# Kernel tuning notes

Hardware: AMD Instinct MI355X
Metric: run time of the kernel (lower is better)

## Reference

```python
import jax, jax.numpy as jnp
import numpy as np

B, S, D = 2, 2048, 2048
H, HKV, HD = 16, 2, 128
THETA = 10000.0


def setup_inputs() -> dict:
    key = jax.random.key(0)
    ks = jax.random.split(key, 5)
    x = jax.random.normal(ks[0], (B, S, D), jnp.float32)
    Wq = jax.random.normal(ks[1], (D, H * HD), jnp.float32) * 0.02
    Wk = jax.random.normal(ks[2], (D, HKV * HD), jnp.float32) * 0.02
    Wv = jax.random.normal(ks[3], (D, HKV * HD), jnp.float32) * 0.02
    Wo = jax.random.normal(ks[4], (H * HD, D), jnp.float32) * 0.02
    mask = jnp.tril(jnp.ones((S, S), jnp.int32))[None, None]  # causal [1,1,S,S]
    return {"x": x, "mask": mask, "Wq": Wq, "Wk": Wk, "Wv": Wv, "Wo": Wo}


def _rope(t, seq_len):
    # t: [B, S, H, HD]; matches RotaryPositionalEmbedding (cos/sin broadcast [S,1,HD])
    inv_freq = 1.0 / (THETA ** (jnp.arange(0, HD, 2, dtype=jnp.float32) / HD))
    pos = jnp.arange(seq_len, dtype=jnp.float32)
    freqs = jnp.einsum('i,j->ij', pos, inv_freq)          # [S, HD/2]
    emb = jnp.concatenate([freqs, freqs], axis=-1)        # [S, HD]
    cos = jnp.cos(emb)[:, None, :]
    sin = jnp.sin(emb)[:, None, :]
    x1, x2 = jnp.split(t, 2, axis=-1)
    rot = jnp.concatenate([-x2, x1], axis=-1)             # rotate_half
    return t * cos + rot * sin


def reference(x, mask, Wq, Wk, Wv, Wo):
    Bx, Sx, _ = x.shape
    q = (x @ Wq).reshape(Bx, Sx, H, HD)
    k = (x @ Wk).reshape(Bx, Sx, HKV, HD)
    v = (x @ Wv).reshape(Bx, Sx, HKV, HD)
    q = _rope(q, Sx)
    k = _rope(k, Sx)
    rep = H // HKV
    # torch .repeat along head dim == tiling (not interleaved)
    k = jnp.tile(k, (1, 1, rep, 1))  # [B, S, H, HD]
    v = jnp.tile(v, (1, 1, rep, 1))
    scale = 1.0 / np.sqrt(HD).astype(np.float32)
    scores = jnp.einsum('bqhd,bkhd->bhqk', q, k) * scale  # [B, H, S, S]
    scores = jnp.where(mask == 0, -jnp.inf, scores)
    attn = jax.nn.softmax(scores.astype(jnp.float32), axis=-1).astype(scores.dtype)
    out = jnp.einsum('bhqk,bkhd->bqhd', attn, v).reshape(Bx, Sx, H * HD)
    return out @ Wo
```

## Files before the change

### kernel.cpp

```cpp
#include <hip/hip_runtime.h>
#include <hip/hip_bf16.h>

#define S_LEN 2048
#define DMODEL 2048
#define NHEAD 16
#define NKVH 2
#define HDIM 128
#define NROW 4096
#define NQKV 2560
#define SCALE 0.08838834764831845f

using short8 = __attribute__((ext_vector_type(8))) short;
using bf16x8 = __attribute__((ext_vector_type(8))) __bf16;
using f32x4  = __attribute__((ext_vector_type(4))) float;

__device__ __forceinline__ f32x4 mfma16(short8 a, short8 b, f32x4 c) {
  return __builtin_amdgcn_mfma_f32_16x16x32_bf16(
      __builtin_bit_cast(bf16x8, a), __builtin_bit_cast(bf16x8, b), c, 0, 0, 0);
}

__device__ __forceinline__ void gload_lds16(const void* g, void* l) {
  __builtin_amdgcn_global_load_lds(
      (const __attribute__((address_space(1))) unsigned int*)g,
      (__attribute__((address_space(3))) unsigned int*)l, 16, 0, 0);
}

__device__ __forceinline__ void storeC(float* C, long idx, float v) { C[idx] = v; }
__device__ __forceinline__ void storeC(__hip_bfloat16* C, long idx, float v) {
  C[idx] = __float2bfloat16(v);
}

__device__ __forceinline__ unsigned short bf16bits(float f) {
  __hip_bfloat16 h = __float2bfloat16(f);
  return *(unsigned short*)&h;
}

__global__ void conv_x(const float* __restrict__ x, __hip_bfloat16* __restrict__ xb) {
  long i = ((long)blockIdx.x * 256 + threadIdx.x) * 4;
  float4 v = *(const float4*)(x + i);
  __hip_bfloat16 o[4];
  o[0] = __float2bfloat16(v.x); o[1] = __float2bfloat16(v.y);
  o[2] = __float2bfloat16(v.z); o[3] = __float2bfloat16(v.w);
  *(ushort4*)(xb + i) = *(const ushort4*)o;
}

__global__ void convT3(const float* __restrict__ Wq, const float* __restrict__ Wk,
                       const float* __restrict__ Wv, __hip_bfloat16* __restrict__ dst) {
  __shared__ float t[32][33];
  int nt = blockIdx.x, kt = blockIdx.y;
  int tx = threadIdx.x, ty = threadIdx.y;
  const float* src; int Ns, n0, row_off;
  if (nt < 64)      { src = Wq; Ns = 2048; n0 = nt * 32;        row_off = n0; }
  else if (nt < 72) { src = Wk; Ns = 256;  n0 = (nt - 64) * 32; row_off = 2048 + n0; }
  else              { src = Wv; Ns = 256;  n0 = (nt - 72) * 32; row_off = 2304 + n0; }
#pragma unroll
  for (int i = 0; i < 4; i++)
    t[ty + i * 8][tx] = src[(long)(kt * 32 + ty + i * 8) * Ns + n0 + tx];
  __syncthreads();
#pragma unroll
  for (int i = 0; i < 4; i++)
    dst[(long)(row_off + ty + i * 8) * 2048 + kt * 32 + tx] =
        __float2bfloat16(t[tx][ty + i * 8]);
}

__global__ void convT(const float* __restrict__ src, __hip_bfloat16* __restrict__ dst,
                      int Ns, int row_off) {
  __shared__ float t[32][33];
  int nt = blockIdx.x, kt = blockIdx.y;
  int tx = threadIdx.x, ty = threadIdx.y;
#pragma unroll
  for (int i = 0; i < 4; i++)
    t[ty + i * 8][tx] = src[(long)(kt * 32 + ty + i * 8) * Ns + nt * 32 + tx];
  __syncthreads();
#pragma unroll
  for (int i = 0; i < 4; i++)
    dst[(long)(row_off + nt * 32 + ty + i * 8) * 2048 + kt * 32 + tx] =
        __float2bfloat16(t[tx][ty + i * 8]);
}

__global__ void mk_table(float* __restrict__ cost, float* __restrict__ sint) {
  int i = blockIdx.x * 256 + threadIdx.x;
  int s = i >> 6, j = i & 63;
  double f = pow(10000.0, -(double)j / 64.0);
  double a = (double)s * f;
  cost[i] = (float)cos(a);
  sint[i] = (float)sin(a);
}

template <typename OutT>
__global__ void gemm_bt(const __hip_bfloat16* __restrict__ A,
                        const __hip_bfloat16* __restrict__ Bt,
                        OutT* __restrict__ C, int M, int N, int K) {
  __shared__ __align__(16) __hip_bfloat16 a_lds[128 * 32];
  __shared__ __align__(16) __hip_bfloat16 b_lds[128 * 32];
  const int tid = threadIdx.x;
  const int wid = tid >> 6, lane = tid & 63;
  const int m0 = blockIdx.y * 128, n0 = blockIdx.x * 128;
  const int wr = wid >> 1, wc = wid & 1;
  const int lrow = lane & 15, lk = lane >> 4;

  const __hip_bfloat16* ag0 = A + (long)(m0 + wid * 16 + (lane >> 2)) * K + (lane & 3) * 8;
  const __hip_bfloat16* bg0 = Bt + (long)(n0 + wid * 16 + (lane >> 2)) * K + (lane & 3) * 8;
  char* al = (char*)a_lds + wid * 1024 + lane * 16;
  char* bl = (char*)b_lds + wid * 1024 + lane * 16;

  f32x4 acc[4][4] = {};

  for (int k0 = 0; k0 < K; k0 += 32) {
    gload_lds16(ag0 + k0, al);
    gload_lds16(ag0 + 64 * (long)K + k0, al + 4096);
    gload_lds16(bg0 + k0, bl);
    gload_lds16(bg0 + 64 * (long)K + k0, bl + 4096);
    __syncthreads();
    short8 af[4], bfr[4];
#pragma unroll
    for (int mi = 0; mi < 4; mi++)
      af[mi] = *(const short8*)(a_lds + (wr * 64 + mi * 16 + lrow) * 32 + lk * 8);
#pragma unroll
    for (int ni = 0; ni < 4; ni++)
      bfr[ni] = *(const short8*)(b_lds + (wc * 64 + ni * 16 + lrow) * 32 + lk * 8);
#pragma unroll
    for (int mi = 0; mi < 4; mi++)
#pragma unroll
      for (int ni = 0; ni < 4; ni++)
        acc[mi][ni] = mfma16(af[mi], bfr[ni], acc[mi][ni]);
    __syncthreads();
  }
#pragma unroll
  for (int mi = 0; mi < 4; mi++)
#pragma unroll
    for (int ni = 0; ni < 4; ni++)
#pragma unroll
      for (int r = 0; r < 4; r++) {
        long row = m0 + wr * 64 + mi * 16 + lk * 4 + r;
        long col = n0 + wc * 64 + ni * 16 + lrow;
        storeC(C, row * N + col, acc[mi][ni][r]);
      }
}

__global__ void rope_kernel(const __hip_bfloat16* __restrict__ qkv,
                            const float* __restrict__ cost, const float* __restrict__ sint,
                            __hip_bfloat16* __restrict__ q_r, __hip_bfloat16* __restrict__ k_t) {
  int tid = threadIdx.x;
  long row = (long)blockIdx.x * 4 + (tid >> 6);
  int j = tid & 63;
  int hh = (int)(row % 18);
  long bs = row / 18;
  int s = (int)(bs & (S_LEN - 1));
  int b = (int)(bs >> 11);
  const __hip_bfloat16* src = qkv + bs * NQKV;
  float c = cost[s * 64 + j], sn = sint[s * 64 + j];
  if (hh < NHEAD) {
    int col0 = hh * HDIM;
    float lo = __bfloat162float(src[col0 + j]);
    float hi = __bfloat162float(src[col0 + j + 64]);
    __hip_bfloat16* dst = q_r + ((long)(b * NHEAD + hh) * S_LEN + s) * HDIM;
    dst[j]      = __float2bfloat16((lo * c - hi * sn) * SCALE);
    dst[j + 64] = __float2bfloat16((hi * c + lo * sn) * SCALE);
  } else {
    int kvh = hh - NHEAD;
    int col0 = DMODEL + kvh * HDIM;
    float lo = __bfloat162float(src[col0 + j]);
    float hi = __bfloat162float(src[col0 + j + 64]);
    long tb = (long)(b * NKVH + kvh) * (S_LEN * HDIM) + (long)(s >> 5) * 4096 +
              (s & 15) * 8 + (j & 7);
    int cs4 = ((s >> 4) & 1) * 4;
    int lkq = ((j >> 3) & 3) * 16;
    int dch = j >> 5;
    k_t[tb + (long)((cs4 + dch) * 64 + lkq) * 8]     = __float2bfloat16(lo * c - hi * sn);
    k_t[tb + (long)((cs4 + dch + 2) * 64 + lkq) * 8] = __float2bfloat16(hi * c + lo * sn);
  }
}

__global__ void vtrans(const __hip_bfloat16* __restrict__ qkv, __hip_bfloat16* __restrict__ v_t) {
  __shared__ __hip_bfloat16 t[32][33];
  int st = blockIdx.x, dt = blockIdx.y, bk = blockIdx.z;
  int tx = threadIdx.x, ty = threadIdx.y;
#pragma unroll
  for (int i = 0; i < 4; i++)
    t[ty + i * 8][tx] = qkv[((long)(bk >> 1) * S_LEN + st * 32 + ty + i * 8) * NQKV +
                            DMODEL + NKVH * HDIM + (bk & 1) * HDIM + dt * 32 + tx];
  __syncthreads();
  long base = (long)bk * (S_LEN * HDIM) + (long)st * 4096 + (tx >> 3) * 128 + (tx & 7);
#pragma unroll
  for (int i = 0; i < 4; i++) {
    int d = dt * 32 + ty + i * 8;
    v_t[base + (long)((d >> 4) * 64 + (d & 15)) * 8] = t[tx][ty + i * 8];
  }
}

__global__ __launch_bounds__(512, 2) void attn_kernel(
    const __hip_bfloat16* __restrict__ q_r, const __hip_bfloat16* __restrict__ k_t,
    const __hip_bfloat16* __restrict__ v_t, __hip_bfloat16* __restrict__ attn_a) {
  __shared__ __align__(16) __hip_bfloat16 k_st[2][4096];
  __shared__ __align__(16) __hip_bfloat16 v_st[2][4096];
  __shared__ __align__(16) __hip_bfloat16 p_lds[8][2 * 16 * 40];
  const int tid = threadIdx.x;
  const int wid = tid >> 6, lane = tid & 63;
  const int lrow = lane & 15, lk = lane >> 4;
  const int bidx = blockIdx.x;
  const int pr = bidx & 31;
  const int hg = (bidx >> 5) & 1;
  const int kv = (bidx >> 6) & 1;
  const int b = bidx >> 7;
  const int myc = (wid < 4) ? pr : (63 - pr);
  const int h = kv + 2 * (hg * 4 + (wid & 3));
  const int q0 = myc * 32;
  const int nkt_w = myc + 1;
  const int nkt_max = 64 - pr;

  const __hip_bfloat16* qb = q_r + (long)(b * NHEAD + h) * S_LEN * HDIM;
  const __hip_bfloat16* kbase = k_t + (long)(b * NKVH + kv) * (S_LEN * HDIM);
  const __hip_bfloat16* vbase = v_t + (long)(b * NKVH + kv) * (S_LEN * HDIM);

  char* kd0 = (char*)&k_st[0][0] + tid * 16;
  char* kd1 = (char*)&k_st[1][0] + tid * 16;
  char* vd0 = (char*)&v_st[0][0] + tid * 16;
  char* vd1 = (char*)&v_st[1][0] + tid * 16;

  short8 qf[2][4];
#pragma unroll
  for (int m = 0; m < 2; m++)
#pragma unroll
    for (int dc = 0; dc < 4; dc++)
      qf[m][dc] = *(const short8*)(qb + (long)(q0 + m * 16 + lrow) * HDIM + dc * 32 + lk * 8);

  f32x4 oacc[2][8] = {};
  float mrow[2] = {4.0f, 4.0f};
  float lsum[2] = {0.f, 0.f};

  gload_lds16(kbase + tid * 8, kd0);
  gload_lds16(vbase + tid * 8, vd0);
  __syncthreads();

  for (int kt = 0; kt < nkt_max; kt++) {
    const char* ks = (const char*)&k_st[kt & 1][0];
    const char* vs = (const char*)&v_st[kt & 1][0];
    if (kt + 1 < nkt_max) {
      gload_lds16(kbase + (long)(kt + 1) * 4096 + tid * 8, (kt & 1) ? kd0 : kd1);
      gload_lds16(vbase + (long)(kt + 1) * 4096 + tid * 8, (kt & 1) ? vd0 : vd1);
    }
    if (kt < nkt_w) {
      const int kc0 = kt * 32;
      short8 kf[2][4];
#pragma unroll
      for (int cs = 0; cs < 2; cs++)
#pragma unroll
        for (int dc = 0; dc < 4; dc++)
          kf[cs][dc] = *(const short8*)(ks + ((cs * 4 + dc) * 64 + lane) * 16);
      f32x4 sacc[2][2] = {};
#pragma unroll
      for (int dc = 0; dc < 4; dc++) {
        sacc[0][0] = mfma16(kf[0][dc], qf[0][dc], sacc[0][0]);
        sacc[0][1] = mfma16(kf[1][dc], qf[0][dc], sacc[0][1]);
        sacc[1][0] = mfma16(kf[0][dc], qf[1][dc], sacc[1][0]);
        sacc[1][1] = mfma16(kf[1][dc], qf[1][dc], sacc[1][1]);
      }
      const bool diag = (kt == nkt_w - 1);
#pragma unroll
      for (int m = 0; m < 2; m++) {
        float pv[8];
#pragma unroll
        for (int cs = 0; cs < 2; cs++)
#pragma unroll
          for (int r = 0; r < 4; r++) pv[cs * 4 + r] = sacc[m][cs][r];
        if (diag) {
          int qrow = q0 + m * 16 + lrow;
#pragma unroll
          for (int cs = 0; cs < 2; cs++)
#pragma unroll
            for (int r = 0; r < 4; r++)
              if (kc0 + cs * 16 + lk * 4 + r > qrow) pv[cs * 4 + r] = -3.0e38f;
        }
        float mx = fmaxf(fmaxf(fmaxf(pv[0], pv[1]), fmaxf(pv[2], pv[3])),
                         fmaxf(fmaxf(pv[4], pv[5]), fmaxf(pv[6], pv[7])));
        if (__builtin_expect(__any(mx > mrow[m] + 8.0f), 0)) {
          float mr = fmaxf(mx, __shfl_xor(mx, 16));
          mr = fmaxf(mr, __shfl_xor(mr, 32));
          float mnew = fmaxf(mrow[m], mr);
          float fr = __expf(mrow[m] - mnew);
          lsum[m] *= fr;
          mrow[m] = mnew;
#pragma unroll
          for (int r2 = 0; r2 < 4; r2++) {
            float fro = __shfl(fr, lk * 4 + r2);
#pragma unroll
            for (int d2 = 0; d2 < 8; d2++) oacc[m][d2][r2] *= fro;
          }
        }
        float pe[8];
#pragma unroll
        for (int i = 0; i < 8; i++) pe[i] = __expf(pv[i] - mrow[m]);
        lsum[m] += ((pe[0] + pe[1]) + (pe[2] + pe[3])) + ((pe[4] + pe[5]) + (pe[6] + pe[7]));
        unsigned short pk[8];
#pragma unroll
        for (int i = 0; i < 8; i++) pk[i] = bf16bits(pe[i]);
        *(ushort4*)(&p_lds[wid][(m * 16 + lrow) * 40 + lk * 4]) = *(ushort4*)&pk[0];
        *(ushort4*)(&p_lds[wid][(m * 16 + lrow) * 40 + 16 + lk * 4]) = *(ushort4*)&pk[4];
      }
      short8 pf[2];
#pragma unroll
      for (int m = 0; m < 2; m++)
        pf[m] = *(const short8*)(&p_lds[wid][(m * 16 + lrow) * 40 + lk * 8]);
#pragma unroll
      for (int d2 = 0; d2 < 8; d2++) {
        short8 vf = *(const short8*)(vs + (d2 * 64 + lane) * 16);
        oacc[0][d2] = mfma16(pf[0], vf, oacc[0][d2]);
        oacc[1][d2] = mfma16(pf[1], vf, oacc[1][d2]);
      }
    }
    __syncthreads();
  }

#pragma unroll
  for (int m = 0; m < 2; m++) {
    float ls = lsum[m];
    ls += __shfl_xor(ls, 16);
    ls += __shfl_xor(ls, 32);
    float inv = 1.0f / ls;
#pragma unroll
    for (int r = 0; r < 4; r++) {
      float invr = __shfl(inv, lk * 4 + r);
      long row = (long)b * S_LEN + q0 + m * 16 + lk * 4 + r;
#pragma unroll
      for (int d2 = 0; d2 < 8; d2++)
        attn_a[row * DMODEL + h * HDIM + d2 * 16 + lrow] =
            __float2bfloat16(oacc[m][d2][r] * invr);
    }
  }
}

extern "C" void kernel_launch(void* const* d_in, const int* in_sizes, int n_in,
                              void* d_out, int out_size, void* d_ws, size_t ws_size,
                              hipStream_t stream) {
  const float* x  = (const float*)d_in[0];
  const float* Wq = (const float*)d_in[2];
  const float* Wk = (const float*)d_in[3];
  const float* Wv = (const float*)d_in[4];
  const float* Wo = (const float*)d_in[5];
  float* out = (float*)d_out;

  char* ws = (char*)d_ws;
  __hip_bfloat16* xb     = (__hip_bfloat16*)(ws + 0);
  __hip_bfloat16* attn_a = xb;
  __hip_bfloat16* wt1    = (__hip_bfloat16*)(ws + 16777216);
  __hip_bfloat16* wto    = (__hip_bfloat16*)(ws + 27262976);
  __hip_bfloat16* qkv    = (__hip_bfloat16*)(ws + 35651584);
  __hip_bfloat16* q_r    = (__hip_bfloat16*)(ws + 56623104);
  __hip_bfloat16* k_t    = (__hip_bfloat16*)(ws + 73400320);
  __hip_bfloat16* v_t    = (__hip_bfloat16*)(ws + 75497472);
  float* cost            = (float*)(ws + 77594624);
  float* sint            = (float*)(ws + 78118912);

  conv_x<<<8192, 256, 0, stream>>>(x, xb);
  convT3<<<dim3(80, 64), dim3(32, 8), 0, stream>>>(Wq, Wk, Wv, wt1);
  convT<<<dim3(64, 64), dim3(32, 8), 0, stream>>>(Wo, wto, 2048, 0);
  mk_table<<<512, 256, 0, stream>>>(cost, sint);

  gemm_bt<__hip_bfloat16><<<dim3(20, 32), 256, 0, stream>>>(xb, wt1, qkv, NROW, NQKV, DMODEL);

  rope_kernel<<<18432, 256, 0, stream>>>(qkv, cost, sint, q_r, k_t);
  vtrans<<<dim3(64, 4, 4), dim3(32, 8), 0, stream>>>(qkv, v_t);

  attn_kernel<<<256, 512, 0, stream>>>(q_r, k_t, v_t, attn_a);

  gemm_bt<float><<<dim3(16, 32), 256, 0, stream>>>(attn_a, wto, out, NROW, DMODEL, DMODEL);
}
```

Measured before the change: 203.1 us.

## Triple-buffer K/V staging in attention and swizzle GEMM block order

The attention kernel moves from a double-buffered K/V LDS pipeline with two barriers per tile to a three-slot ring. It prefetches two tiles ahead and uses explicit vmcnt waits plus a single barrier per iteration, so more load latency is hidden behind compute. Separately, the GEMM kernel remaps its linear block index in groups of 8 to change the tile order across workgroups, likely to improve L2/cache locality across XCDs. The extra LDS buffer raises shared memory use, which could limit occupancy at 2 blocks per CU. The hand-written waitcnt logic depends on exactly two loads being outstanding per stage.

```diff
diff --git a/kernel.cpp b/kernel.cpp
--- a/kernel.cpp
+++ b/kernel.cpp
@@ -95,7 +95,11 @@
   __shared__ __align__(16) __hip_bfloat16 b_lds[128 * 32];
   const int tid = threadIdx.x;
   const int wid = tid >> 6, lane = tid & 63;
-  const int m0 = blockIdx.y * 128, n0 = blockIdx.x * 128;
+  const int nbx = gridDim.x;
+  int bid = blockIdx.y * nbx + blockIdx.x;
+  const int nwg = nbx * gridDim.y;
+  bid = (bid & 7) * (nwg >> 3) + (bid >> 3);
+  const int m0 = (bid / nbx) * 128, n0 = (bid % nbx) * 128;
   const int wr = wid >> 1, wc = wid & 1;
   const int lrow = lane & 15, lk = lane >> 4;
 
@@ -192,9 +196,9 @@
 __global__ __launch_bounds__(512, 2) void attn_kernel(
     const __hip_bfloat16* __restrict__ q_r, const __hip_bfloat16* __restrict__ k_t,
     const __hip_bfloat16* __restrict__ v_t, __hip_bfloat16* __restrict__ attn_a) {
-  __shared__ __align__(16) __hip_bfloat16 k_st[2][4096];
-  __shared__ __align__(16) __hip_bfloat16 v_st[2][4096];
-  __shared__ __align__(16) __hip_bfloat16 p_lds[8][2 * 16 * 40];
+  __shared__ __align__(16) __hip_bfloat16 k_st[3][4096];
+  __shared__ __align__(16) __hip_bfloat16 v_st[3][4096];
+  __shared__ __align__(16) __hip_bfloat16 p_lds[8][32 * 40];
   const int tid = threadIdx.x;
   const int wid = tid >> 6, lane = tid & 63;
   const int lrow = lane & 15, lk = lane >> 4;
@@ -207,16 +211,16 @@
   const int h = kv + 2 * (hg * 4 + (wid & 3));
   const int q0 = myc * 32;
   const int nkt_w = myc + 1;
-  const int nkt_max = 64 - pr;
+  const int NV = 64 - pr;
 
   const __hip_bfloat16* qb = q_r + (long)(b * NHEAD + h) * S_LEN * HDIM;
   const __hip_bfloat16* kbase = k_t + (long)(b * NKVH + kv) * (S_LEN * HDIM);
   const __hip_bfloat16* vbase = v_t + (long)(b * NKVH + kv) * (S_LEN * HDIM);
 
-  char* kd0 = (char*)&k_st[0][0] + tid * 16;
-  char* kd1 = (char*)&k_st[1][0] + tid * 16;
-  char* vd0 = (char*)&v_st[0][0] + tid * 16;
-  char* vd1 = (char*)&v_st[1][0] + tid * 16;
+  auto stage = [&](int tile, int bi) {
+    gload_lds16(kbase + (long)tile * 4096 + tid * 8, (char*)&k_st[bi][0] + tid * 16);
+    gload_lds16(vbase + (long)tile * 4096 + tid * 8, (char*)&v_st[bi][0] + tid * 16);
+  };
 
   short8 qf[2][4];
 #pragma unroll
@@ -229,19 +233,26 @@
   float mrow[2] = {4.0f, 4.0f};
   float lsum[2] = {0.f, 0.f};
 
-  gload_lds16(kbase + tid * 8, kd0);
-  gload_lds16(vbase + tid * 8, vd0);
-  __syncthreads();
-
-  for (int kt = 0; kt < nkt_max; kt++) {
-    const char* ks = (const char*)&k_st[kt & 1][0];
-    const char* vs = (const char*)&v_st[kt & 1][0];
-    if (kt + 1 < nkt_max) {
-      gload_lds16(kbase + (long)(kt + 1) * 4096 + tid * 8, (kt & 1) ? kd0 : kd1);
-      gload_lds16(vbase + (long)(kt + 1) * 4096 + tid * 8, (kt & 1) ? vd0 : vd1);
+  stage(0, 0);
+  stage(1 < NV ? 1 : 0, 1);
+  int bi = 0;
+  for (int vt = 0; vt < NV; vt++) {
+    if (vt + 1 < NV) {
+      asm volatile("s_waitcnt vmcnt(2)" ::: "memory");
+    } else {
+      asm volatile("s_waitcnt vmcnt(0)" ::: "memory");
     }
-    if (kt < nkt_w) {
-      const int kc0 = kt * 32;
+    __builtin_amdgcn_s_barrier();
+    if (vt + 2 < NV) {
+      int b2 = bi + 2; if (b2 >= 3) b2 -= 3;
+      stage(vt + 2, b2);
+    }
+    if (vt < nkt_w) {
+      const char* ks = (const char*)&k_st[bi][0];
+      const char* vs = (const char*)&v_st[bi][0];
+      const int kc0 = vt * 32;
+      const bool diag = (vt == nkt_w - 1);
+
       short8 kf[2][4];
 #pragma unroll
       for (int cs = 0; cs < 2; cs++)
@@ -256,7 +267,6 @@
         sacc[1][0] = mfma16(kf[0][dc], qf[1][dc], sacc[1][0]);
         sacc[1][1] = mfma16(kf[1][dc], qf[1][dc], sacc[1][1]);
       }
-      const bool diag = (kt == nkt_w - 1);
 #pragma unroll
       for (int m = 0; m < 2; m++) {
         float pv[8];
@@ -309,7 +319,7 @@
         oacc[1][d2] = mfma16(pf[1], vf, oacc[1][d2]);
       }
     }
-    __syncthreads();
+    bi = bi + 1; if (bi >= 3) bi -= 3;
   }
 
 #pragma unroll
```

Result: slower. 217.1 us (+6.9%).

## Double attention KV tile to 64 keys and swizzle GEMM block order

Applied to the files above, without the earlier changes.

The attention kernel now stages 64-key K/V tiles (two 32-key sub-tiles) per iteration, which halves the number of loop iterations and __syncthreads barriers and amortizes softmax bookkeeping over more columns. Diagonal masking now works at 64-key granularity, so the diagonal tile can hold more masked wasted work. LDS use doubles, which may reduce occupancy. Separately, the GEMM remaps block IDs in groups of 8 so that concurrently scheduled blocks fall in a different pattern, likely aimed at spreading work across the XCDs or improving L2 reuse.

```diff
diff --git a/kernel.cpp b/kernel.cpp
--- a/kernel.cpp
+++ b/kernel.cpp
@@ -95,7 +95,11 @@
   __shared__ __align__(16) __hip_bfloat16 b_lds[128 * 32];
   const int tid = threadIdx.x;
   const int wid = tid >> 6, lane = tid & 63;
-  const int m0 = blockIdx.y * 128, n0 = blockIdx.x * 128;
+  const int nbx = gridDim.x;
+  int bid = blockIdx.y * nbx + blockIdx.x;
+  const int nwg = nbx * gridDim.y;
+  bid = (bid & 7) * (nwg >> 3) + (bid >> 3);
+  const int m0 = (bid / nbx) * 128, n0 = (bid % nbx) * 128;
   const int wr = wid >> 1, wc = wid & 1;
   const int lrow = lane & 15, lk = lane >> 4;
 
@@ -192,9 +196,9 @@
 __global__ __launch_bounds__(512, 2) void attn_kernel(
     const __hip_bfloat16* __restrict__ q_r, const __hip_bfloat16* __restrict__ k_t,
     const __hip_bfloat16* __restrict__ v_t, __hip_bfloat16* __restrict__ attn_a) {
-  __shared__ __align__(16) __hip_bfloat16 k_st[2][4096];
-  __shared__ __align__(16) __hip_bfloat16 v_st[2][4096];
-  __shared__ __align__(16) __hip_bfloat16 p_lds[8][2 * 16 * 40];
+  __shared__ __align__(16) __hip_bfloat16 k_st[2][8192];
+  __shared__ __align__(16) __hip_bfloat16 v_st[2][8192];
+  __shared__ __align__(16) unsigned short p_lds[8][32 * 72];
   const int tid = threadIdx.x;
   const int wid = tid >> 6, lane = tid & 63;
   const int lrow = lane & 15, lk = lane >> 4;
@@ -206,17 +210,21 @@
   const int myc = (wid < 4) ? pr : (63 - pr);
   const int h = kv + 2 * (hg * 4 + (wid & 3));
   const int q0 = myc * 32;
-  const int nkt_w = myc + 1;
-  const int nkt_max = 64 - pr;
+  const int nkt_w = (myc >> 1) + 1;
+  const int NV = ((63 - pr) >> 1) + 1;
 
   const __hip_bfloat16* qb = q_r + (long)(b * NHEAD + h) * S_LEN * HDIM;
   const __hip_bfloat16* kbase = k_t + (long)(b * NKVH + kv) * (S_LEN * HDIM);
   const __hip_bfloat16* vbase = v_t + (long)(b * NKVH + kv) * (S_LEN * HDIM);
 
-  char* kd0 = (char*)&k_st[0][0] + tid * 16;
-  char* kd1 = (char*)&k_st[1][0] + tid * 16;
-  char* vd0 = (char*)&v_st[0][0] + tid * 16;
-  char* vd1 = (char*)&v_st[1][0] + tid * 16;
+  auto stage = [&](int t, int bi) {
+    const __hip_bfloat16* kg = kbase + (long)t * 8192;
+    const __hip_bfloat16* vg = vbase + (long)t * 8192;
+    gload_lds16(kg + tid * 8,        (char*)&k_st[bi][0] + tid * 16);
+    gload_lds16(kg + 4096 + tid * 8, (char*)&k_st[bi][4096] + tid * 16);
+    gload_lds16(vg + tid * 8,        (char*)&v_st[bi][0] + tid * 16);
+    gload_lds16(vg + 4096 + tid * 8, (char*)&v_st[bi][4096] + tid * 16);
+  };
 
   short8 qf[2][4];
 #pragma unroll
@@ -229,51 +237,48 @@
   float mrow[2] = {4.0f, 4.0f};
   float lsum[2] = {0.f, 0.f};
 
-  gload_lds16(kbase + tid * 8, kd0);
-  gload_lds16(vbase + tid * 8, vd0);
+  stage(0, 0);
   __syncthreads();
-
-  for (int kt = 0; kt < nkt_max; kt++) {
-    const char* ks = (const char*)&k_st[kt & 1][0];
-    const char* vs = (const char*)&v_st[kt & 1][0];
-    if (kt + 1 < nkt_max) {
-      gload_lds16(kbase + (long)(kt + 1) * 4096 + tid * 8, (kt & 1) ? kd0 : kd1);
-      gload_lds16(vbase + (long)(kt + 1) * 4096 + tid * 8, (kt & 1) ? vd0 : vd1);
-    }
+  for (int kt = 0; kt < NV; kt++) {
+    if (kt + 1 < NV) stage(kt + 1, (kt + 1) & 1);
     if (kt < nkt_w) {
-      const int kc0 = kt * 32;
-      short8 kf[2][4];
-#pragma unroll
-      for (int cs = 0; cs < 2; cs++)
+      const __hip_bfloat16* ks = &k_st[kt & 1][0];
+      const __hip_bfloat16* vs = &v_st[kt & 1][0];
+      const int kc0 = kt * 64;
+      const bool diag = (kt == nkt_w - 1);
+
+      f32x4 sacc[2][4] = {};
+#pragma unroll
+      for (int ks4 = 0; ks4 < 4; ks4++) {
+        const __hip_bfloat16* kst = ks + (ks4 >> 1) * 4096;
+        short8 kf[4];
 #pragma unroll
         for (int dc = 0; dc < 4; dc++)
-          kf[cs][dc] = *(const short8*)(ks + ((cs * 4 + dc) * 64 + lane) * 16);
-      f32x4 sacc[2][2] = {};
-#pragma unroll
-      for (int dc = 0; dc < 4; dc++) {
-        sacc[0][0] = mfma16(kf[0][dc], qf[0][dc], sacc[0][0]);
-        sacc[0][1] = mfma16(kf[1][dc], qf[0][dc], sacc[0][1]);
-        sacc[1][0] = mfma16(kf[0][dc], qf[1][dc], sacc[1][0]);
-        sacc[1][1] = mfma16(kf[1][dc], qf[1][dc], sacc[1][1]);
+          kf[dc] = *(const short8*)(kst + (((ks4 & 1) * 4 + dc) * 64 + lane) * 8);
+#pragma unroll
+        for (int dc = 0; dc < 4; dc++) {
+          sacc[0][ks4] = mfma16(kf[dc], qf[0][dc], sacc[0][ks4]);
+          sacc[1][ks4] = mfma16(kf[dc], qf[1][dc], sacc[1][ks4]);
+        }
       }
-      const bool diag = (kt == nkt_w - 1);
 #pragma unroll
       for (int m = 0; m < 2; m++) {
-        float pv[8];
-#pragma unroll
-        for (int cs = 0; cs < 2; cs++)
-#pragma unroll
-          for (int r = 0; r < 4; r++) pv[cs * 4 + r] = sacc[m][cs][r];
+        float pv[16];
+#pragma unroll
+        for (int ks4 = 0; ks4 < 4; ks4++)
+#pragma unroll
+          for (int r = 0; r < 4; r++) pv[ks4 * 4 + r] = sacc[m][ks4][r];
         if (diag) {
           int qrow = q0 + m * 16 + lrow;
 #pragma unroll
-          for (int cs = 0; cs < 2; cs++)
+          for (int ks4 = 0; ks4 < 4; ks4++)
 #pragma unroll
             for (int r = 0; r < 4; r++)
-              if (kc0 + cs * 16 + lk * 4 + r > qrow) pv[cs * 4 + r] = -3.0e38f;
+              if (kc0 + ks4 * 16 + lk * 4 + r > qrow) pv[ks4 * 4 + r] = -3.0e38f;
         }
-        float mx = fmaxf(fmaxf(fmaxf(pv[0], pv[1]), fmaxf(pv[2], pv[3])),
-                         fmaxf(fmaxf(pv[4], pv[5]), fmaxf(pv[6], pv[7])));
+        float mx = pv[0];
+#pragma unroll
+        for (int i = 1; i < 16; i++) mx = fmaxf(mx, pv[i]);
         if (__builtin_expect(__any(mx > mrow[m] + 8.0f), 0)) {
           float mr = fmaxf(mx, __shfl_xor(mx, 16));
           mr = fmaxf(mr, __shfl_xor(mr, 32));
@@ -288,25 +293,35 @@
             for (int d2 = 0; d2 < 8; d2++) oacc[m][d2][r2] *= fro;
           }
         }
-        float pe[8];
-#pragma unroll
-        for (int i = 0; i < 8; i++) pe[i] = __expf(pv[i] - mrow[m]);
-        lsum[m] += ((pe[0] + pe[1]) + (pe[2] + pe[3])) + ((pe[4] + pe[5]) + (pe[6] + pe[7]));
-        unsigned short pk[8];
-#pragma unroll
-        for (int i = 0; i < 8; i++) pk[i] = bf16bits(pe[i]);
-        *(ushort4*)(&p_lds[wid][(m * 16 + lrow) * 40 + lk * 4]) = *(ushort4*)&pk[0];
-        *(ushort4*)(&p_lds[wid][(m * 16 + lrow) * 40 + 16 + lk * 4]) = *(ushort4*)&pk[4];
+        float ls = 0.f;
+        unsigned short pk[16];
+#pragma unroll
+        for (int i = 0; i < 16; i++) {
+          float e = __expf(pv[i] - mrow[m]);
+          ls += e;
+          pk[i] = bf16bits(e);
+        }
+        lsum[m] += ls;
+        unsigned short* prow = &p_lds[wid][(m * 16 + lrow) * 72];
+        *(ushort4*)(prow + lk * 4)      = *(ushort4*)&pk[0];
+        *(ushort4*)(prow + 16 + lk * 4) = *(ushort4*)&pk[4];
+        *(ushort4*)(prow + 32 + lk * 4) = *(ushort4*)&pk[8];
+        *(ushort4*)(prow + 48 + lk * 4) = *(ushort4*)&pk[12];
       }
-      short8 pf[2];
+      short8 pf[2][2];
 #pragma unroll
       for (int m = 0; m < 2; m++)
-        pf[m] = *(const short8*)(&p_lds[wid][(m * 16 + lrow) * 40 + lk * 8]);
+#pragma unroll
+        for (int hf = 0; hf < 2; hf++)
+          pf[m][hf] = *(const short8*)(&p_lds[wid][(m * 16 + lrow) * 72 + hf * 32 + lk * 8]);
 #pragma unroll
       for (int d2 = 0; d2 < 8; d2++) {
-        short8 vf = *(const short8*)(vs + (d2 * 64 + lane) * 16);
-        oacc[0][d2] = mfma16(pf[0], vf, oacc[0][d2]);
-        oacc[1][d2] = mfma16(pf[1], vf, oacc[1][d2]);
+        short8 vf0 = *(const short8*)(vs + (d2 * 64 + lane) * 8);
+        short8 vf1 = *(const short8*)(vs + 4096 + (d2 * 64 + lane) * 8);
+        oacc[0][d2] = mfma16(pf[0][0], vf0, oacc[0][d2]);
+        oacc[1][d2] = mfma16(pf[1][0], vf0, oacc[1][d2]);
+        oacc[0][d2] = mfma16(pf[0][1], vf1, oacc[0][d2]);
+        oacc[1][d2] = mfma16(pf[1][1], vf1, oacc[1][d2]);
       }
     }
     __syncthreads();
```

New measurement: 205.7 us. No clear change (+1.3%).

## Split attention into per-chunk 256-thread blocks and swizzle GEMM tile order

Applied to the files above, without the earlier changes.

The attention kernel no longer pairs a short and a long causal query chunk inside one 512-thread block. It now launches 512 blocks of 4 waves, each handling a single query chunk and looping only over the key tiles that chunk needs. This drops the idle iterations where the short-chunk waves waited at barriers for the long-chunk waves, at the cost of a more uneven load per block and K/V tiles staged by fewer threads. Separately, the GEMM remaps block IDs in an XCD-aware interleaved order so that neighbouring tiles land on the same chiplet, aiming for better L2 reuse.

```diff
diff --git a/kernel.cpp b/kernel.cpp
--- a/kernel.cpp
+++ b/kernel.cpp
@@ -95,7 +95,11 @@
   __shared__ __align__(16) __hip_bfloat16 b_lds[128 * 32];
   const int tid = threadIdx.x;
   const int wid = tid >> 6, lane = tid & 63;
-  const int m0 = blockIdx.y * 128, n0 = blockIdx.x * 128;
+  const int nbx = gridDim.x;
+  int bid = blockIdx.y * nbx + blockIdx.x;
+  const int nwg = nbx * gridDim.y;
+  bid = (bid & 7) * (nwg >> 3) + (bid >> 3);
+  const int m0 = (bid / nbx) * 128, n0 = (bid % nbx) * 128;
   const int wr = wid >> 1, wc = wid & 1;
   const int lrow = lane & 15, lk = lane >> 4;
 
@@ -189,34 +193,39 @@
   }
 }
 
-__global__ __launch_bounds__(512, 2) void attn_kernel(
+__global__ __launch_bounds__(256, 2) void attn_kernel(
     const __hip_bfloat16* __restrict__ q_r, const __hip_bfloat16* __restrict__ k_t,
     const __hip_bfloat16* __restrict__ v_t, __hip_bfloat16* __restrict__ attn_a) {
   __shared__ __align__(16) __hip_bfloat16 k_st[2][4096];
   __shared__ __align__(16) __hip_bfloat16 v_st[2][4096];
-  __shared__ __align__(16) __hip_bfloat16 p_lds[8][2 * 16 * 40];
+  __shared__ __align__(16) unsigned short p_lds[4][32 * 40];
   const int tid = threadIdx.x;
   const int wid = tid >> 6, lane = tid & 63;
   const int lrow = lane & 15, lk = lane >> 4;
   const int bidx = blockIdx.x;
-  const int pr = bidx & 31;
-  const int hg = (bidx >> 5) & 1;
-  const int kv = (bidx >> 6) & 1;
-  const int b = bidx >> 7;
-  const int myc = (wid < 4) ? pr : (63 - pr);
-  const int h = kv + 2 * (hg * 4 + (wid & 3));
-  const int q0 = myc * 32;
-  const int nkt_w = myc + 1;
-  const int nkt_max = 64 - pr;
+  const int half = bidx >> 8;
+  const int r5 = bidx & 255;
+  const int b = r5 >> 7;
+  const int kv = (r5 >> 6) & 1;
+  const int hg = (r5 >> 5) & 1;
+  const int j = r5 & 31;
+  const int c = half ? (63 - j) : j;
+  const int h = kv + 2 * (hg * 4 + wid);
+  const int q0 = c * 32;
+  const int nkt = c + 1;
 
   const __hip_bfloat16* qb = q_r + (long)(b * NHEAD + h) * S_LEN * HDIM;
   const __hip_bfloat16* kbase = k_t + (long)(b * NKVH + kv) * (S_LEN * HDIM);
   const __hip_bfloat16* vbase = v_t + (long)(b * NKVH + kv) * (S_LEN * HDIM);
 
-  char* kd0 = (char*)&k_st[0][0] + tid * 16;
-  char* kd1 = (char*)&k_st[1][0] + tid * 16;
-  char* vd0 = (char*)&v_st[0][0] + tid * 16;
-  char* vd1 = (char*)&v_st[1][0] + tid * 16;
+  auto stage = [&](int t, int bi) {
+    const __hip_bfloat16* kg = kbase + (long)t * 4096;
+    const __hip_bfloat16* vg = vbase + (long)t * 4096;
+    gload_lds16(kg + tid * 8,        (char*)&k_st[bi][0] + tid * 16);
+    gload_lds16(kg + 2048 + tid * 8, (char*)&k_st[bi][2048] + tid * 16);
+    gload_lds16(vg + tid * 8,        (char*)&v_st[bi][0] + tid * 16);
+    gload_lds16(vg + 2048 + tid * 8, (char*)&v_st[bi][2048] + tid * 16);
+  };
 
   short8 qf[2][4];
 #pragma unroll
@@ -229,85 +238,79 @@
   float mrow[2] = {4.0f, 4.0f};
   float lsum[2] = {0.f, 0.f};
 
-  gload_lds16(kbase + tid * 8, kd0);
-  gload_lds16(vbase + tid * 8, vd0);
+  stage(0, 0);
   __syncthreads();
-
-  for (int kt = 0; kt < nkt_max; kt++) {
-    const char* ks = (const char*)&k_st[kt & 1][0];
-    const char* vs = (const char*)&v_st[kt & 1][0];
-    if (kt + 1 < nkt_max) {
-      gload_lds16(kbase + (long)(kt + 1) * 4096 + tid * 8, (kt & 1) ? kd0 : kd1);
-      gload_lds16(vbase + (long)(kt + 1) * 4096 + tid * 8, (kt & 1) ? vd0 : vd1);
+  for (int kt = 0; kt < nkt; kt++) {
+    if (kt + 1 < nkt) stage(kt + 1, (kt + 1) & 1);
+    const __hip_bfloat16* ks = &k_st[kt & 1][0];
+    const __hip_bfloat16* vs = &v_st[kt & 1][0];
+    const int kc0 = kt * 32;
+    const bool diag = (kt == nkt - 1);
+
+    short8 kf[2][4];
+#pragma unroll
+    for (int cs = 0; cs < 2; cs++)
+#pragma unroll
+      for (int dc = 0; dc < 4; dc++)
+        kf[cs][dc] = *(const short8*)(ks + ((cs * 4 + dc) * 64 + lane) * 8);
+    f32x4 sacc[2][2] = {};
+#pragma unroll
+    for (int dc = 0; dc < 4; dc++) {
+      sacc[0][0] = mfma16(kf[0][dc], qf[0][dc], sacc[0][0]);
+      sacc[0][1] = mfma16(kf[1][dc], qf[0][dc], sacc[0][1]);
+      sacc[1][0] = mfma16(kf[0][dc], qf[1][dc], sacc[1][0]);
+      sacc[1][1] = mfma16(kf[1][dc], qf[1][dc], sacc[1][1]);
     }
-    if (kt < nkt_w) {
-      const int kc0 = kt * 32;
-      short8 kf[2][4];
+#pragma unroll
+    for (int m = 0; m < 2; m++) {
+      float pv[8];
 #pragma unroll
       for (int cs = 0; cs < 2; cs++)
 #pragma unroll
-        for (int dc = 0; dc < 4; dc++)
-          kf[cs][dc] = *(const short8*)(ks + ((cs * 4 + dc) * 64 + lane) * 16);
-      f32x4 sacc[2][2] = {};
-#pragma unroll
-      for (int dc = 0; dc < 4; dc++) {
-        sacc[0][0] = mfma16(kf[0][dc], qf[0][dc], sacc[0][0]);
-        sacc[0][1] = mfma16(kf[1][dc], qf[0][dc], sacc[0][1]);
-        sacc[1][0] = mfma16(kf[0][dc], qf[1][dc], sacc[1][0]);
-        sacc[1][1] = mfma16(kf[1][dc], qf[1][dc], sacc[1][1]);
+        for (int r = 0; r < 4; r++) pv[cs * 4 + r] = sacc[m][cs][r];
+      if (diag) {
+        int qrow = q0 + m * 16 + lrow;
+#pragma unroll
+        for (int cs = 0; cs < 2; cs++)
+#pragma unroll
+          for (int r = 0; r < 4; r++)
+            if (kc0 + cs * 16 + lk * 4 + r > qrow) pv[cs * 4 + r] = -3.0e38f;
       }
-      const bool diag = (kt == nkt_w - 1);
-#pragma unroll
-      for (int m = 0; m < 2; m++) {
-        float pv[8];
-#pragma unroll
-        for (int cs = 0; cs < 2; cs++)
-#pragma unroll
-          for (int r = 0; r < 4; r++) pv[cs * 4 + r] = sacc[m][cs][r];
-        if (diag) {
-          int qrow = q0 + m * 16 + lrow;
-#pragma unroll
-          for (int cs = 0; cs < 2; cs++)
-#pragma unroll
-            for (int r = 0; r < 4; r++)
-              if (kc0 + cs * 16 + lk * 4 + r > qrow) pv[cs * 4 + r] = -3.0e38f;
+      float mx = fmaxf(fmaxf(fmaxf(pv[0], pv[1]), fmaxf(pv[2], pv[3])),
+                       fmaxf(fmaxf(pv[4], pv[5]), fmaxf(pv[6], pv[7])));
+      if (__builtin_expect(__any(mx > mrow[m] + 8.0f), 0)) {
+        float mr = fmaxf(mx, __shfl_xor(mx, 16));
+        mr = fmaxf(mr, __shfl_xor(mr, 32));
+        float mnew = fmaxf(mrow[m], mr);
+        float fr = __expf(mrow[m] - mnew);
+        lsum[m] *= fr;
+        mrow[m] = mnew;
+#pragma unroll
+        for (int r2 = 0; r2 < 4; r2++) {
+          float fro = __shfl(fr, lk * 4 + r2);
+#pragma unroll
+          for (int d2 = 0; d2 < 8; d2++) oacc[m][d2][r2] *= fro;
         }
-        float mx = fmaxf(fmaxf(fmaxf(pv[0], pv[1]), fmaxf(pv[2], pv[3])),
-                         fmaxf(fmaxf(pv[4], pv[5]), fmaxf(pv[6], pv[7])));
-        if (__builtin_expect(__any(mx > mrow[m] + 8.0f), 0)) {
-          float mr = fmaxf(mx, __shfl_xor(mx, 16));
-          mr = fmaxf(mr, __shfl_xor(mr, 32));
-          float mnew = fmaxf(mrow[m], mr);
-          float fr = __expf(mrow[m] - mnew);
-          lsum[m] *= fr;
-          mrow[m] = mnew;
-#pragma unroll
-          for (int r2 = 0; r2 < 4; r2++) {
-            float fro = __shfl(fr, lk * 4 + r2);
-#pragma unroll
-            for (int d2 = 0; d2 < 8; d2++) oacc[m][d2][r2] *= fro;
-          }
-        }
-        float pe[8];
-#pragma unroll
-        for (int i = 0; i < 8; i++) pe[i] = __expf(pv[i] - mrow[m]);
-        lsum[m] += ((pe[0] + pe[1]) + (pe[2] + pe[3])) + ((pe[4] + pe[5]) + (pe[6] + pe[7]));
-        unsigned short pk[8];
-#pragma unroll
-        for (int i = 0; i < 8; i++) pk[i] = bf16bits(pe[i]);
-        *(ushort4*)(&p_lds[wid][(m * 16 + lrow) * 40 + lk * 4]) = *(ushort4*)&pk[0];
-        *(ushort4*)(&p_lds[wid][(m * 16 + lrow) * 40 + 16 + lk * 4]) = *(ushort4*)&pk[4];
       }
-      short8 pf[2];
-#pragma unroll
-      for (int m = 0; m < 2; m++)
-        pf[m] = *(const short8*)(&p_lds[wid][(m * 16 + lrow) * 40 + lk * 8]);
-#pragma unroll
-      for (int d2 = 0; d2 < 8; d2++) {
-        short8 vf = *(const short8*)(vs + (d2 * 64 + lane) * 16);
-        oacc[0][d2] = mfma16(pf[0], vf, oacc[0][d2]);
-        oacc[1][d2] = mfma16(pf[1], vf, oacc[1][d2]);
-      }
+      float pe[8];
+#pragma unroll
+      for (int i = 0; i < 8; i++) pe[i] = __expf(pv[i] - mrow[m]);
+      lsum[m] += ((pe[0] + pe[1]) + (pe[2] + pe[3])) + ((pe[4] + pe[5]) + (pe[6] + pe[7]));
+      unsigned short pk[8];
+#pragma unroll
+      for (int i = 0; i < 8; i++) pk[i] = bf16bits(pe[i]);
+      *(ushort4*)(&p_lds[wid][(m * 16 + lrow) * 40 + lk * 4]) = *(ushort4*)&pk[0];
+      *(ushort4*)(&p_lds[wid][(m * 16 + lrow) * 40 + 16 + lk * 4]) = *(ushort4*)&pk[4];
+    }
+    short8 pf[2];
+#pragma unroll
+    for (int m = 0; m < 2; m++)
+      pf[m] = *(const short8*)(&p_lds[wid][(m * 16 + lrow) * 40 + lk * 8]);
+#pragma unroll
+    for (int d2 = 0; d2 < 8; d2++) {
+      short8 vf = *(const short8*)(vs + (d2 * 64 + lane) * 8);
+      oacc[0][d2] = mfma16(pf[0], vf, oacc[0][d2]);
+      oacc[1][d2] = mfma16(pf[1], vf, oacc[1][d2]);
     }
     __syncthreads();
   }
@@ -362,7 +365,7 @@
   rope_kernel<<<18432, 256, 0, stream>>>(qkv, cost, sint, q_r, k_t);
   vtrans<<<dim3(64, 4, 4), dim3(32, 8), 0, stream>>>(qkv, v_t);
 
-  attn_kernel<<<256, 512, 0, stream>>>(q_r, k_t, v_t, attn_a);
+  attn_kernel<<<512, 256, 0, stream>>>(q_r, k_t, v_t, attn_a);
 
   gemm_bt<float><<<dim3(16, 32), 256, 0, stream>>>(attn_a, wto, out, NROW, DMODEL, DMODEL);
 }
```

New measurement: 215.8 us. 6.3% more time.
